# Kernel optimization log

Hardware: AMD Instinct MI355X
Metric: run time of the kernel (lower is better)

Reference implementation:

```python
import jax, jax.numpy as jnp
import numpy as np

TWO_PI = 2.0 * np.pi


def setup_inputs() -> dict:
    key = jax.random.key(0)
    ks = jax.random.split(key, 6)
    n1 = n2 = n3 = 20
    nk, ni, nspin = 4, 16, 2
    # Invertible, physically plausible lattice (~8 Bohr cubic cell + jitter)
    A = jnp.eye(3, dtype=jnp.float32) * 8.0 + 0.05 * jax.random.normal(ks[0], (3, 3), jnp.float32)
    k_grid = 0.1 * jax.random.normal(ks[1], (nk, 3), jnp.float32)
    cg_real = jax.random.normal(ks[2], (nspin, nk, ni, n1, n2, n3), jnp.float32)
    cg_imag = jax.random.normal(ks[3], (nspin, nk, ni, n1, n2, n3), jnp.float32)
    # Real-space evaluation grid: fractional coords in [0,1)^3 mapped through A
    frac = jax.random.uniform(ks[4], (n1, n2, n3, 3), jnp.float32)
    r = frac @ A
    return {"A": A, "k_grid": k_grid, "cg_real": cg_real, "cg_imag": cg_imag, "r": r}


def reference(A, k_grid, cg_real, cg_imag, r):
    # cg: [spin, nk, ni, n1, n2, n3] complex plane-wave coefficients
    cg = cg_real + 1j * cg_imag
    n1, n2, n3 = cg.shape[-3:]
    # Integer FFT frequency mesh m -> reciprocal-lattice vectors G = m @ B,
    # B rows are reciprocal basis: B = 2*pi * inv(A)^T  (A rows = lattice vecs)
    f1 = jnp.fft.fftfreq(n1) * n1
    f2 = jnp.fft.fftfreq(n2) * n2
    f3 = jnp.fft.fftfreq(n3) * n3
    m = jnp.stack(jnp.meshgrid(f1, f2, f3, indexing="ij"), axis=-1).astype(A.dtype)  # [n1,n2,n3,3]
    B = TWO_PI * jnp.linalg.inv(A).T
    G = (m @ B).reshape(-1, 3)                      # [nG, 3]
    vol = jnp.abs(jnp.linalg.det(A))
    Rf = r.reshape(-1, 3)                           # [nR, 3]
    # Plane-wave synthesis: psi_{s,k,i}(r) = exp(i k.r)/sqrt(vol) * sum_G c_G exp(i G.r)
    # (equivalent to the triple-nested vmap over the grid dims, fully vectorized)
    phase_g = jnp.exp(1j * (Rf @ G.T))              # [nR, nG] complex
    dens = cg.reshape(*cg.shape[:3], -1)            # [spin, nk, ni, nG]
    psi = jnp.einsum("skin,rn->skir", dens, phase_g)  # [spin, nk, ni, nR]
    phase_k = jnp.exp(1j * (Rf @ k_grid.T))         # [nR, nk]
    psi = psi * jnp.moveaxis(phase_k, 0, -1)[None, :, None, :]
    psi = psi / jnp.sqrt(vol).astype(psi.real.dtype)
    # [spin, nk, ni, n1, n2, n3] -- matches moveaxis(range(3), range(-3,0))
    return psi.reshape(*cg.shape[:3], *r.shape[:-1])
```

## Files before the change

### kernel.cpp

```cpp
#include <hip/hip_runtime.h>

typedef __attribute__((ext_vector_type(4))) float f32x4;
typedef __attribute__((ext_vector_type(8))) short s16x8;

#define NG     8000
#define NRPT   8000
#define NSKIN  128
#define NT     64
#define KCH    800
#define NKC    10
#define NTILES 25
#define NROUND 10
#define NSLOT  6
#define TPB    256
#define WS_TILE_B 16384
#define WS_NEED   ((size_t)NKC*NTILES*WS_TILE_B)

__device__ __forceinline__ float sin_rev(float u){ float r; asm("v_sin_f32 %0, %1" : "=v"(r) : "v"(u)); return r; }
__device__ __forceinline__ float cos_rev(float u){ float r; asm("v_cos_f32 %0, %1" : "=v"(r) : "v"(u)); return r; }
__device__ __forceinline__ unsigned int cvt_pk(float lo, float hi){
    unsigned int r; asm("v_cvt_pk_bf16_f32 %0, %1, %2" : "=v"(r) : "v"(lo), "v"(hi)); return r;
}
__device__ __forceinline__ s16x8 bneg(s16x8 v){
    int4 u = *(int4*)&v;
    u.x ^= 0x80008000; u.y ^= 0x80008000; u.z ^= 0x80008000; u.w ^= 0x80008000;
    return *(s16x8*)&u;
}
__device__ __forceinline__ s16x8 pack8(float4 v0, float4 v1){
    union { s16x8 v; uint4 u; } r;
    r.u.x = cvt_pk(v0.x,v0.y); r.u.y = cvt_pk(v0.z,v0.w);
    r.u.z = cvt_pk(v1.x,v1.y); r.u.w = cvt_pk(v1.z,v1.w);
    return r.v;
}
__device__ __forceinline__ int swz(int row, int kg){
    return row*64 + ((kg ^ ((row>>1)&3))<<4);
}

__global__ __launch_bounds__(256) void bloch_prepass(
    const float* __restrict__ cgr, const float* __restrict__ cgi,
    char* __restrict__ ws)
{
    int gid = blockIdx.x*256 + threadIdx.x;
    if (gid >= NKC*NTILES*2*8*64) return;
    int lane  = gid & 63;
    int rb8   = (gid >> 6) & 7;
    int plane = (gid >> 9) & 1;
    int tile  = gid >> 10;
    int row   = rb8*16 + (lane & 15);
    int k     = tile*32 + (lane >> 4)*8;
    const float* src = plane ? cgi : cgr;
    const float4 v0 = *(const float4*)&src[(size_t)row*NG + k];
    const float4 v1 = *(const float4*)&src[(size_t)row*NG + k + 4];
    uint4 p;
    p.x = cvt_pk(v0.x, v0.y); p.y = cvt_pk(v0.z, v0.w);
    p.z = cvt_pk(v1.x, v1.y); p.w = cvt_pk(v1.z, v1.w);
    *(uint4*)(ws + (size_t)gid*16) = p;
}

template<bool PRE>
__global__ __launch_bounds__(TPB, 3) void bloch14(
    const float* __restrict__ Amat, const float* __restrict__ kgrid,
    const float* __restrict__ cgr,  const float* __restrict__ cgi,
    const float* __restrict__ rpts, const char* __restrict__ ws,
    float* __restrict__ out, int out_size)
{
    __shared__ __align__(16) char smem[NSLOT*8192];
    __shared__ float fracS[NT][4];
    __shared__ float invAS[9];
    __shared__ float scaleS;

    const int tid = threadIdx.x;
    const int bid = blockIdx.x;
    const int kc  = bid >> 8;
    const int idx = bid & 255;
    const int rb  = idx >> 1;
    const int mb  = idx & 1;
    if (rb >= 125) return;
    const int r_base = rb * NT;

    if (tid == 0) {
        float a00=Amat[0],a01=Amat[1],a02=Amat[2];
        float a10=Amat[3],a11=Amat[4],a12=Amat[5];
        float a20=Amat[6],a21=Amat[7],a22=Amat[8];
        float c00 =  (a11*a22 - a12*a21);
        float c01 = -(a10*a22 - a12*a20);
        float c02 =  (a10*a21 - a11*a20);
        float det = a00*c00 + a01*c01 + a02*c02;
        float id  = 1.0f/det;
        invAS[0] =  c00*id;
        invAS[1] = -(a01*a22 - a02*a21)*id;
        invAS[2] =  (a01*a12 - a02*a11)*id;
        invAS[3] =  c01*id;
        invAS[4] =  (a00*a22 - a02*a20)*id;
        invAS[5] = -(a00*a12 - a02*a10)*id;
        invAS[6] =  c02*id;
        invAS[7] = -(a00*a21 - a01*a20)*id;
        invAS[8] =  (a00*a11 - a01*a10)*id;
        scaleS   = rsqrtf(fabsf(det));
    }
    __syncthreads();

    if (tid < NT) {
        int rg = r_base + tid;
        float r0 = rpts[rg*3+0], r1 = rpts[rg*3+1], r2 = rpts[rg*3+2];
        fracS[tid][0] = r0*invAS[0] + r1*invAS[3] + r2*invAS[6];
        fracS[tid][1] = r0*invAS[1] + r1*invAS[4] + r2*invAS[7];
        fracS[tid][2] = r0*invAS[2] + r1*invAS[5] + r2*invAS[8];
    }
    __syncthreads();

    f32x4 accRe[2][2], accIm[2][2];
    #pragma unroll
    for (int mi = 0; mi < 2; ++mi)
        #pragma unroll
        for (int ni = 0; ni < 2; ++ni) {
            accRe[mi][ni] = (f32x4){0.f,0.f,0.f,0.f};
            accIm[mi][ni] = (f32x4){0.f,0.f,0.f,0.f};
        }

    const int lane = tid & 63;
    const int wid  = tid >> 6;
    const int wm   = wid >> 1;
    const int wn   = wid & 1;
    const int frow = lane & 15;
    const int kq   = lane >> 4;
    const int bOff = swz(wn*32 + frow, kq);

    const float f0r = fracS[lane][0], f1r = fracS[lane][1], f2r = fracS[lane][2];
    float u1 = f2r - floorf(f2r);
    const float w1c = cos_rev(u1), w1s = sin_rev(u1);
    float yd = -20.0f * f2r; yd -= floorf(yd);
    const float wdc = cos_rev(yd), wds = sin_rev(yd);
    const float w1wdc = w1c*wdc - w1s*wds;
    const float w1wds = w1c*wds + w1s*wdc;

    auto stageRing = [&](int R){
        int i12 = kc*40 + 4*R + wid;
        int i1  = (i12 * 3277) >> 16;
        int i2  = i12 - i1*20;
        float m1 = (float)(i1 - (i1 >= 10 ? 20 : 0));
        float m2 = (float)(i2 - (i2 >= 10 ? 20 : 0));
        float y0 = m1*f0r + m2*f1r; y0 -= floorf(y0);
        float cc = cos_rev(y0), cs = sin_rev(y0);
        unsigned int pkc[10], pks[10];
        #pragma unroll
        for (int jj = 0; jj < 10; ++jj) {
            float ac = cc, as_ = cs;
            { float nc = cc*w1c - cs*w1s, ns = cc*w1s + cs*w1c; cc=nc; cs=ns; }
            pkc[jj] = cvt_pk(ac, cc);
            pks[jj] = cvt_pk(as_, cs);
            if (jj < 9) {
                if (jj == 4) { float nc = cc*w1wdc - cs*w1wds, ns = cc*w1wds + cs*w1wdc; cc=nc; cs=ns; }
                else         { float nc = cc*w1c  - cs*w1s,  ns = cc*w1s  + cs*w1c;  cc=nc; cs=ns; }
            }
        }
        int gg = (80*R + wid*20) % 192;
        int gA = gg >> 3;
        auto adr = [&](int g, int p)->char* {
            if (g >= 24) g -= 24;
            return smem + (g>>2)*8192 + p*4096 + swz(lane, g&3);
        };
        if ((gg & 7) == 0) {
            *(uint4*)adr(gA,0)   = make_uint4(pkc[0],pkc[1],pkc[2],pkc[3]);
            *(uint4*)adr(gA+1,0) = make_uint4(pkc[4],pkc[5],pkc[6],pkc[7]);
            *(uint2*)adr(gA+2,0) = make_uint2(pkc[8],pkc[9]);
            *(uint4*)adr(gA,1)   = make_uint4(pks[0],pks[1],pks[2],pks[3]);
            *(uint4*)adr(gA+1,1) = make_uint4(pks[4],pks[5],pks[6],pks[7]);
            *(uint2*)adr(gA+2,1) = make_uint2(pks[8],pks[9]);
        } else {
            *(uint2*)(adr(gA,0)+8) = make_uint2(pkc[0],pkc[1]);
            *(uint4*)adr(gA+1,0)   = make_uint4(pkc[2],pkc[3],pkc[4],pkc[5]);
            *(uint4*)adr(gA+2,0)   = make_uint4(pkc[6],pkc[7],pkc[8],pkc[9]);
            *(uint2*)(adr(gA,1)+8) = make_uint2(pks[0],pks[1]);
            *(uint4*)adr(gA+1,1)   = make_uint4(pks[2],pks[3],pks[4],pks[5]);
            *(uint4*)adr(gA+2,1)   = make_uint4(pks[6],pks[7],pks[8],pks[9]);
        }
    };

    s16x8 arfP[2], aifP[2];
    auto loadA = [&](int t){
        if (PRE) {
            const char* tb = ws + (size_t)(kc*NTILES + t)*WS_TILE_B + lane*16;
            #pragma unroll
            for (int mi = 0; mi < 2; ++mi) {
                arfP[mi] = *(const s16x8*)(tb +        (mb*4 + wm*2 + mi)*1024);
                aifP[mi] = *(const s16x8*)(tb + 8192 + (mb*4 + wm*2 + mi)*1024);
            }
        } else {
            #pragma unroll
            for (int mi = 0; mi < 2; ++mi) {
                int row = mb*64 + wm*32 + mi*16 + frow;
                int k   = kc*KCH + t*32 + kq*8;
                const float* pr_ = &cgr[(size_t)row*NG + k];
                const float* pi_ = &cgi[(size_t)row*NG + k];
                arfP[mi] = pack8(*(const float4*)pr_, *(const float4*)(pr_+4));
                aifP[mi] = pack8(*(const float4*)pi_, *(const float4*)(pi_+4));
            }
        }
    };

    loadA(0);
    stageRing(0);
    __syncthreads();

    int tcur = 0, slot = 0;
    #pragma unroll 1
    for (int R = 0; R < NROUND; ++R) {
        if (R + 1 < NROUND) stageRing(R + 1);
        const int t_hi = (5*R + 5) >> 1;
        #pragma unroll 1
        while (tcur < t_hi) {
            const char* base = smem + slot*8192;
            s16x8 bcf[2], bsf[2], bsnf[2];
            #pragma unroll
            for (int ni = 0; ni < 2; ++ni) {
                bcf[ni]  = *(const s16x8*)(base +        bOff + ni*1024);
                bsf[ni]  = *(const s16x8*)(base + 4096 + bOff + ni*1024);
                bsnf[ni] = bneg(bsf[ni]);
            }
            __builtin_amdgcn_s_setprio(1);
            #pragma unroll
            for (int mi = 0; mi < 2; ++mi)
                #pragma unroll
                for (int ni = 0; ni < 2; ++ni) {
                    accRe[mi][ni] = __builtin_amdgcn_mfma_f32_16x16x32_bf16(arfP[mi], bcf[ni],  accRe[mi][ni], 0, 0, 0);
                    accRe[mi][ni] = __builtin_amdgcn_mfma_f32_16x16x32_bf16(aifP[mi], bsnf[ni], accRe[mi][ni], 0, 0, 0);
                    accIm[mi][ni] = __builtin_amdgcn_mfma_f32_16x16x32_bf16(arfP[mi], bsf[ni],  accIm[mi][ni], 0, 0, 0);
                    accIm[mi][ni] = __builtin_amdgcn_mfma_f32_16x16x32_bf16(aifP[mi], bcf[ni],  accIm[mi][ni], 0, 0, 0);
                }
            __builtin_amdgcn_s_setprio(0);
            ++tcur;
            if (tcur < NTILES) loadA(tcur);
            ++slot; if (slot == NSLOT) slot = 0;
        }
        __syncthreads();
    }

    float2* ekr = (float2*)smem;
    {
        int col = tid >> 2, kidx = tid & 3;
        int rg = r_base + col;
        float r0 = rpts[rg*3+0], r1 = rpts[rg*3+1], r2 = rpts[rg*3+2];
        float ang = (r0*kgrid[kidx*3+0] + r1*kgrid[kidx*3+1] + r2*kgrid[kidx*3+2])
                    * 0.15915494309189535f;
        float u = ang - floorf(ang);
        ekr[col*4+kidx] = make_float2(cos_rev(u), sin_rev(u));
    }
    __syncthreads();

    const bool write_imag = (out_size >= 2*NSKIN*NRPT);
    const float scale = scaleS;
    #pragma unroll
    for (int mi = 0; mi < 2; ++mi) {
        const int m0 = mb*64 + wm*32 + mi*16;
        const int kidx = (m0 >> 4) & 3;
        #pragma unroll
        for (int ni = 0; ni < 2; ++ni) {
            int col = wn*32 + ni*16 + frow;
            int rg = r_base + col;
            float2 e = ekr[col*4+kidx];
            float ck = e.x, sk = e.y;
            #pragma unroll
            for (int v = 0; v < 4; ++v) {
                int sg = m0 + kq*4 + v;
                float re = accRe[mi][ni][v];
                float im = accIm[mi][ni][v];
                float orr = (re*ck - im*sk) * scale;
                size_t lin = (size_t)sg * NRPT + rg;
                if (write_imag) {
                    float oi = (re*sk + im*ck) * scale;
                    size_t idx2 = lin * 2;
                    if (idx2 + 1 < (size_t)out_size) {
                        atomicAdd(&out[idx2],   orr);
                        atomicAdd(&out[idx2+1], oi);
                    }
                } else {
                    atomicAdd(&out[lin], orr);
                }
            }
        }
    }
}

extern "C" void kernel_launch(void* const* d_in, const int* in_sizes, int n_in,
                              void* d_out, int out_size, void* d_ws, size_t ws_size,
                              hipStream_t stream) {
    const float* Amat  = (const float*)d_in[0];
    const float* kgrid = (const float*)d_in[1];
    const float* cgr   = (const float*)d_in[2];
    const float* cgi   = (const float*)d_in[3];
    const float* rpts  = (const float*)d_in[4];
    float* out = (float*)d_out;

    hipMemsetAsync(d_out, 0, (size_t)out_size * sizeof(float), stream);

    const bool use_pre = (ws_size >= WS_NEED);
    dim3 grid(NKC * 256);
    if (use_pre) {
        bloch_prepass<<<dim3(NKC*NTILES*2*8*64/256), 256, 0, stream>>>(cgr, cgi, (char*)d_ws);
        bloch14<true><<<grid, TPB, 0, stream>>>(Amat, kgrid, cgr, cgi, rpts,
                                                (const char*)d_ws, out, out_size);
    } else {
        bloch14<false><<<grid, TPB, 0, stream>>>(Amat, kgrid, cgr, cgi, rpts,
                                                 nullptr, out, out_size);
    }
}
```

Before: 92.02 us.

## Switch to 32x32x16 MFMA and cover all 128 rows per block

Replaces the 16x16x32 bf16 MFMA tiling with 32x32x16 MFMAs and makes each block cover all 128 spin/k/band rows instead of splitting them across two blocks. This halves the grid, so the per-block cos/sin phase staging into shared memory is no longer computed twice for the same r-block. The prepass layout and the epilogue index mapping are rewritten to match the new MFMA fragment layout. In exchange, register pressure rises, occupancy drops to 2 blocks per CU, and there are fewer blocks to spread across the CUs.

```diff
diff --git a/kernel.cpp b/kernel.cpp
--- a/kernel.cpp
+++ b/kernel.cpp
@@ -1,6 +1,6 @@
 #include <hip/hip_runtime.h>
 
-typedef __attribute__((ext_vector_type(4))) float f32x4;
+typedef __attribute__((ext_vector_type(16))) float f32x16;
 typedef __attribute__((ext_vector_type(8))) short s16x8;
 
 #define NG     8000
@@ -26,12 +26,6 @@
     u.x ^= 0x80008000; u.y ^= 0x80008000; u.z ^= 0x80008000; u.w ^= 0x80008000;
     return *(s16x8*)&u;
 }
-__device__ __forceinline__ s16x8 pack8(float4 v0, float4 v1){
-    union { s16x8 v; uint4 u; } r;
-    r.u.x = cvt_pk(v0.x,v0.y); r.u.y = cvt_pk(v0.z,v0.w);
-    r.u.z = cvt_pk(v1.x,v1.y); r.u.w = cvt_pk(v1.z,v1.w);
-    return r.v;
-}
 __device__ __forceinline__ int swz(int row, int kg){
     return row*64 + ((kg ^ ((row>>1)&3))<<4);
 }
@@ -43,11 +37,12 @@
     int gid = blockIdx.x*256 + threadIdx.x;
     if (gid >= NKC*NTILES*2*8*64) return;
     int lane  = gid & 63;
-    int rb8   = (gid >> 6) & 7;
+    int c     = (gid >> 6) & 7;
     int plane = (gid >> 9) & 1;
     int tile  = gid >> 10;
-    int row   = rb8*16 + (lane & 15);
-    int k     = tile*32 + (lane >> 4)*8;
+    int wm = c >> 2, mp = (c >> 1) & 1, kh = c & 1;
+    int row = wm*64 + mp*32 + (lane & 31);
+    int k   = tile*32 + kh*16 + (lane >> 5)*8;
     const float* src = plane ? cgi : cgr;
     const float4 v0 = *(const float4*)&src[(size_t)row*NG + k];
     const float4 v1 = *(const float4*)&src[(size_t)row*NG + k + 4];
@@ -58,7 +53,7 @@
 }
 
 template<bool PRE>
-__global__ __launch_bounds__(TPB, 3) void bloch14(
+__global__ __launch_bounds__(TPB, 2) void bloch16(
     const float* __restrict__ Amat, const float* __restrict__ kgrid,
     const float* __restrict__ cgr,  const float* __restrict__ cgi,
     const float* __restrict__ rpts, const char* __restrict__ ws,
@@ -71,10 +66,8 @@
 
     const int tid = threadIdx.x;
     const int bid = blockIdx.x;
-    const int kc  = bid >> 8;
-    const int idx = bid & 255;
-    const int rb  = idx >> 1;
-    const int mb  = idx & 1;
+    const int kc  = bid >> 7;
+    const int rb  = bid & 127;
     if (rb >= 125) return;
     const int r_base = rb * NT;
 
@@ -109,22 +102,22 @@
     }
     __syncthreads();
 
-    f32x4 accRe[2][2], accIm[2][2];
+    f32x16 accRe[2], accIm[2];
     #pragma unroll
-    for (int mi = 0; mi < 2; ++mi)
-        #pragma unroll
-        for (int ni = 0; ni < 2; ++ni) {
-            accRe[mi][ni] = (f32x4){0.f,0.f,0.f,0.f};
-            accIm[mi][ni] = (f32x4){0.f,0.f,0.f,0.f};
-        }
+    for (int mp = 0; mp < 2; ++mp) {
+        #pragma unroll
+        for (int e = 0; e < 16; ++e) { accRe[mp][e] = 0.f; accIm[mp][e] = 0.f; }
+    }
 
     const int lane = tid & 63;
     const int wid  = tid >> 6;
     const int wm   = wid >> 1;
     const int wn   = wid & 1;
-    const int frow = lane & 15;
-    const int kq   = lane >> 4;
-    const int bOff = swz(wn*32 + frow, kq);
+    const int colL = wn*32 + (lane & 31);
+    const int hB   = lane >> 5;
+
+    const int bOff0 = swz(colL, 0*2 + hB);
+    const int bOff1 = swz(colL, 1*2 + hB);
 
     const float f0r = fracS[lane][0], f1r = fracS[lane][1], f2r = fracS[lane][2];
     float u1 = f2r - floorf(f2r);
@@ -177,29 +170,38 @@
         }
     };
 
-    s16x8 arfP[2], aifP[2];
+    s16x8 arf[2][2], aif[2][2];
     auto loadA = [&](int t){
-        if (PRE) {
-            const char* tb = ws + (size_t)(kc*NTILES + t)*WS_TILE_B + lane*16;
+        const char* tb = ws + (size_t)(kc*NTILES + t)*WS_TILE_B + lane*16;
+        #pragma unroll
+        for (int mp = 0; mp < 2; ++mp)
             #pragma unroll
-            for (int mi = 0; mi < 2; ++mi) {
-                arfP[mi] = *(const s16x8*)(tb +        (mb*4 + wm*2 + mi)*1024);
-                aifP[mi] = *(const s16x8*)(tb + 8192 + (mb*4 + wm*2 + mi)*1024);
-            }
-        } else {
+            for (int kh = 0; kh < 2; ++kh) {
+                arf[mp][kh] = *(const s16x8*)(tb +        (wm*4 + mp*2 + kh)*1024);
+                aif[mp][kh] = *(const s16x8*)(tb + 8192 + (wm*4 + mp*2 + kh)*1024);
+            }
+    };
+    auto loadA_direct = [&](int t){
+        #pragma unroll
+        for (int mp = 0; mp < 2; ++mp)
             #pragma unroll
-            for (int mi = 0; mi < 2; ++mi) {
-                int row = mb*64 + wm*32 + mi*16 + frow;
-                int k   = kc*KCH + t*32 + kq*8;
+            for (int kh = 0; kh < 2; ++kh) {
+                int row = wm*64 + mp*32 + (lane & 31);
+                int k   = kc*KCH + t*32 + kh*16 + hB*8;
                 const float* pr_ = &cgr[(size_t)row*NG + k];
                 const float* pi_ = &cgi[(size_t)row*NG + k];
-                arfP[mi] = pack8(*(const float4*)pr_, *(const float4*)(pr_+4));
-                aifP[mi] = pack8(*(const float4*)pi_, *(const float4*)(pi_+4));
-            }
-        }
+                float4 r0 = *(const float4*)pr_, r1 = *(const float4*)(pr_+4);
+                float4 i0 = *(const float4*)pi_, i1 = *(const float4*)(pi_+4);
+                union { s16x8 v; uint4 u; } pr, pi;
+                pr.u = make_uint4(cvt_pk(r0.x,r0.y), cvt_pk(r0.z,r0.w),
+                                  cvt_pk(r1.x,r1.y), cvt_pk(r1.z,r1.w));
+                pi.u = make_uint4(cvt_pk(i0.x,i0.y), cvt_pk(i0.z,i0.w),
+                                  cvt_pk(i1.x,i1.y), cvt_pk(i1.z,i1.w));
+                arf[mp][kh] = pr.v; aif[mp][kh] = pi.v;
+            }
     };
 
-    loadA(0);
+    if (PRE) loadA(0); else loadA_direct(0);
     stageRing(0);
     __syncthreads();
 
@@ -212,25 +214,26 @@
         while (tcur < t_hi) {
             const char* base = smem + slot*8192;
             s16x8 bcf[2], bsf[2], bsnf[2];
-            #pragma unroll
-            for (int ni = 0; ni < 2; ++ni) {
-                bcf[ni]  = *(const s16x8*)(base +        bOff + ni*1024);
-                bsf[ni]  = *(const s16x8*)(base + 4096 + bOff + ni*1024);
-                bsnf[ni] = bneg(bsf[ni]);
-            }
+            bcf[0] = *(const s16x8*)(base +        bOff0);
+            bcf[1] = *(const s16x8*)(base +        bOff1);
+            bsf[0] = *(const s16x8*)(base + 4096 + bOff0);
+            bsf[1] = *(const s16x8*)(base + 4096 + bOff1);
+            bsnf[0] = bneg(bsf[0]); bsnf[1] = bneg(bsf[1]);
             __builtin_amdgcn_s_setprio(1);
             #pragma unroll
-            for (int mi = 0; mi < 2; ++mi)
-                #pragma unroll
-                for (int ni = 0; ni < 2; ++ni) {
-                    accRe[mi][ni] = __builtin_amdgcn_mfma_f32_16x16x32_bf16(arfP[mi], bcf[ni],  accRe[mi][ni], 0, 0, 0);
-                    accRe[mi][ni] = __builtin_amdgcn_mfma_f32_16x16x32_bf16(aifP[mi], bsnf[ni], accRe[mi][ni], 0, 0, 0);
-                    accIm[mi][ni] = __builtin_amdgcn_mfma_f32_16x16x32_bf16(arfP[mi], bsf[ni],  accIm[mi][ni], 0, 0, 0);
-                    accIm[mi][ni] = __builtin_amdgcn_mfma_f32_16x16x32_bf16(aifP[mi], bcf[ni],  accIm[mi][ni], 0, 0, 0);
-                }
+            for (int kh = 0; kh < 2; ++kh) {
+                accRe[0] = __builtin_amdgcn_mfma_f32_32x32x16_bf16(arf[0][kh], bcf[kh],  accRe[0], 0, 0, 0);
+                accRe[1] = __builtin_amdgcn_mfma_f32_32x32x16_bf16(arf[1][kh], bcf[kh],  accRe[1], 0, 0, 0);
+                accIm[0] = __builtin_amdgcn_mfma_f32_32x32x16_bf16(arf[0][kh], bsf[kh],  accIm[0], 0, 0, 0);
+                accIm[1] = __builtin_amdgcn_mfma_f32_32x32x16_bf16(arf[1][kh], bsf[kh],  accIm[1], 0, 0, 0);
+                accRe[0] = __builtin_amdgcn_mfma_f32_32x32x16_bf16(aif[0][kh], bsnf[kh], accRe[0], 0, 0, 0);
+                accRe[1] = __builtin_amdgcn_mfma_f32_32x32x16_bf16(aif[1][kh], bsnf[kh], accRe[1], 0, 0, 0);
+                accIm[0] = __builtin_amdgcn_mfma_f32_32x32x16_bf16(aif[0][kh], bcf[kh],  accIm[0], 0, 0, 0);
+                accIm[1] = __builtin_amdgcn_mfma_f32_32x32x16_bf16(aif[1][kh], bcf[kh],  accIm[1], 0, 0, 0);
+            }
             __builtin_amdgcn_s_setprio(0);
             ++tcur;
-            if (tcur < NTILES) loadA(tcur);
+            if (tcur < NTILES) { if (PRE) loadA(tcur); else loadA_direct(tcur); }
             ++slot; if (slot == NSLOT) slot = 0;
         }
         __syncthreads();
@@ -250,21 +253,21 @@
 
     const bool write_imag = (out_size >= 2*NSKIN*NRPT);
     const float scale = scaleS;
+    const int rg = r_base + colL;
     #pragma unroll
-    for (int mi = 0; mi < 2; ++mi) {
-        const int m0 = mb*64 + wm*32 + mi*16;
-        const int kidx = (m0 >> 4) & 3;
-        #pragma unroll
-        for (int ni = 0; ni < 2; ++ni) {
-            int col = wn*32 + ni*16 + frow;
-            int rg = r_base + col;
-            float2 e = ekr[col*4+kidx];
+    for (int mp = 0; mp < 2; ++mp) {
+        #pragma unroll
+        for (int q = 0; q < 4; ++q) {
+            const int kidx = mp*2 + (q >> 1);
+            float2 e = ekr[colL*4 + kidx];
             float ck = e.x, sk = e.y;
             #pragma unroll
-            for (int v = 0; v < 4; ++v) {
-                int sg = m0 + kq*4 + v;
-                float re = accRe[mi][ni][v];
-                float im = accIm[mi][ni][v];
+            for (int rr = 0; rr < 4; ++rr) {
+                const int reg = q*4 + rr;
+                int row = rr + 8*q + 4*hB;
+                int sg  = wm*64 + mp*32 + row;
+                float re = accRe[mp][reg];
+                float im = accIm[mp][reg];
                 float orr = (re*ck - im*sk) * scale;
                 size_t lin = (size_t)sg * NRPT + rg;
                 if (write_imag) {
@@ -295,13 +298,13 @@
     hipMemsetAsync(d_out, 0, (size_t)out_size * sizeof(float), stream);
 
     const bool use_pre = (ws_size >= WS_NEED);
-    dim3 grid(NKC * 256);
+    dim3 grid(NKC * 128);
     if (use_pre) {
         bloch_prepass<<<dim3(NKC*NTILES*2*8*64/256), 256, 0, stream>>>(cgr, cgi, (char*)d_ws);
-        bloch14<true><<<grid, TPB, 0, stream>>>(Amat, kgrid, cgr, cgi, rpts,
+        bloch16<true><<<grid, TPB, 0, stream>>>(Amat, kgrid, cgr, cgi, rpts,
                                                 (const char*)d_ws, out, out_size);
     } else {
-        bloch14<false><<<grid, TPB, 0, stream>>>(Amat, kgrid, cgr, cgi, rpts,
+        bloch16<false><<<grid, TPB, 0, stream>>>(Amat, kgrid, cgr, cgi, rpts,
                                                  nullptr, out, out_size);
     }
 }
```

New measurement: 94.42 us. +2.6%, slower.
